# Kernel optimization log

Hardware: AMD Instinct MI355X
Metric: run time of the kernel (lower is better)

Reference implementation:

```python
import jax, jax.numpy as jnp
import numpy as np
from jax import lax

MASK_EPS = 1e-45  # matches torch (mask + 1e-45).log()

B, N, L, T = 32, 64, 64, 10
V, D, H = 50257, 256, 512


def setup_inputs() -> dict:
    key = jax.random.key(0)
    ks = jax.random.split(key, 10)
    s = 0.02
    return {
        "sents": jax.random.randint(ks[0], (B, N, L), 0, V),
        "titles": jax.random.randint(ks[1], (B, N, T), 0, V),
        "emb": jax.random.normal(ks[2], (V, D), jnp.float32) * s,
        "Wt": jax.random.normal(ks[3], (D, H), jnp.float32) * s,
        "bt": jnp.zeros((H,), jnp.float32),
        "W_ih": jax.random.normal(ks[4], (D, 3 * H), jnp.float32) * s,
        "W_hh": jax.random.normal(ks[5], (H, 3 * H), jnp.float32) * s,
        "b_ih": jnp.zeros((3 * H,), jnp.float32),
        "b_hh": jnp.zeros((3 * H,), jnp.float32),
        "W_att_in": jax.random.normal(ks[6], (H, H), jnp.float32) * s,
        "W_att_out": jax.random.normal(ks[7], (2 * H, H), jnp.float32) * s,
        "b_att_out": jnp.zeros((H,), jnp.float32),
    }


def reference(sents, titles, emb, Wt, bt, W_ih, W_hh, b_ih, b_hh,
              W_att_in, W_att_out, b_att_out):
    # embedding gather + per-sentence bag-of-words sum  [B,N,D]
    x = emb[sents].sum(axis=2)
    # title -> initial sentence-level hidden (t2h), titles[:,0,:-2] summed
    h0 = emb[titles[:, 0]].sum(axis=1) @ Wt + bt            # [B,H]

    def gru_step(h, xi):
        gi = xi @ W_ih + b_ih                               # [B,3H]
        gh = h @ W_hh + b_hh
        ir, iz, inn = jnp.split(gi, 3, axis=-1)
        hr, hz, hn = jnp.split(gh, 3, axis=-1)
        r = jax.nn.sigmoid(ir + hr)
        z = jax.nn.sigmoid(iz + hz)
        n = jnp.tanh(inn + r * hn)
        h_new = (1.0 - z) * n + z * h
        return h_new, h_new

    _, hs = lax.scan(gru_step, h0, jnp.swapaxes(x, 0, 1))   # [N,B,H]
    hs = jnp.swapaxes(hs, 0, 1)                             # [B,N,H]

    # GlobalAttention over the growing stack of hs with incremental mask
    # == causal attention over sentence hidden states
    q = hs @ W_att_in                                       # [B,N,H]
    align = jnp.einsum('bqh,bkh->bqk', q, hs)               # [B,N,N]
    causal = jnp.tril(jnp.ones((N, N), jnp.float32))
    align = align + jnp.log(causal + MASK_EPS)
    a = jax.nn.softmax(align, axis=-1)
    c = jnp.einsum('bqk,bkh->bqh', a, hs)                   # [B,N,H]
    attn_h = jnp.tanh(jnp.concatenate([c, hs], axis=-1) @ W_att_out + b_att_out)
    return attn_h
```

## Files before the change

### kernel.cpp

```cpp
#include <hip/hip_runtime.h>
#include <hip/hip_bf16.h>

constexpr int cB = 32, cN = 64, cL = 64, cT = 10, cD = 256, cH = 512, cH3 = 1536;
constexpr int cBN = cB * cN;
constexpr int cNP1 = cN + 1;

typedef __bf16 bf16x8 __attribute__((ext_vector_type(8)));
typedef float f32x4 __attribute__((ext_vector_type(4)));

__device__ __forceinline__ ushort f2bf(float f) {
  __hip_bfloat16 h = __float2bfloat16(f);
  return *reinterpret_cast<ushort*>(&h);
}

__global__ void k_embed_x(const int* __restrict__ sents, const float* __restrict__ emb,
                          ushort* __restrict__ xb) {
  __shared__ int idx[cL];
  int bn = blockIdx.x, t = threadIdx.x;
  if (t < cL) idx[t] = sents[bn * cL + t];
  __syncthreads();
  float acc = 0.f;
#pragma unroll 8
  for (int l = 0; l < cL; ++l) acc += emb[(long)idx[l] * cD + t];
  xb[bn * cD + t] = f2bf(acc);
}

__global__ void k_title(const int* __restrict__ titles, const float* __restrict__ emb,
                        float* __restrict__ tsum) {
  __shared__ int idx[cT];
  int b = blockIdx.x, t = threadIdx.x;
  if (t < cT) idx[t] = titles[b * cN * cT + t];
  __syncthreads();
  float acc = 0.f;
#pragma unroll
  for (int i = 0; i < cT; ++i) acc += emb[(long)idx[i] * cD + t];
  tsum[b * cD + t] = acc;
}

__global__ void k_h0(const float* __restrict__ tsum, const float* __restrict__ Wt,
                     const float* __restrict__ bt, float* __restrict__ hse) {
  int i = blockIdx.x * blockDim.x + threadIdx.x;
  int b = i >> 9, hh = i & (cH - 1);
  const float* ts = tsum + b * cD;
  float acc = bt[hh];
  for (int k = 0; k < cD; ++k) acc += ts[k] * Wt[(long)k * cH + hh];
  hse[(long)b * cNP1 * cH + hh] = acc;
}

__global__ void k_bti(const float* __restrict__ W, ushort* __restrict__ Bt) {
  __shared__ float tile[64][65];
  int col0 = blockIdx.x * 64, k0 = blockIdx.y * 64;
  int t = threadIdx.x;
  for (int i = t; i < 4096; i += 256) {
    int kr = i >> 6, cc = i & 63;
    tile[kr][cc] = W[(long)(k0 + kr) * cH3 + col0 + cc];
  }
  __syncthreads();
  for (int i = t; i < 4096; i += 256) {
    int cc = i >> 6, kr = i & 63;
    Bt[(long)(col0 + cc) * cD + k0 + kr] = f2bf(tile[kr][cc]);
  }
}

__global__ void k_bq(const float* __restrict__ W, ushort* __restrict__ Bt) {
  __shared__ float tile[64][65];
  int col0 = blockIdx.x * 64, k0 = blockIdx.y * 64;
  int t = threadIdx.x;
  for (int i = t; i < 4096; i += 256) {
    int kr = i >> 6, cc = i & 63;
    tile[kr][cc] = W[(long)(k0 + kr) * cH + col0 + cc];
  }
  __syncthreads();
  for (int i = t; i < 4096; i += 256) {
    int cc = i >> 6, kr = i & 63;
    Bt[(long)(col0 + cc) * cH + k0 + kr] = f2bf(tile[kr][cc]);
  }
}

__global__ void __launch_bounds__(256) k_gi_mfma(
    const ushort* __restrict__ xb, const ushort* __restrict__ Bt,
    const float* __restrict__ b_ih, float* __restrict__ gi) {
  __shared__ char lds[16384];
  int bn0 = blockIdx.x * 64, col0 = blockIdx.y * 64;
  int t = threadIdx.x;
  int w = t >> 6, lane = t & 63;
  f32x4 acc[4];
#pragma unroll
  for (int i = 0; i < 4; ++i) acc[i] = (f32x4){0.f, 0.f, 0.f, 0.f};
  int r = lane & 15, kg = lane >> 4;
  for (int kc = 0; kc < 4; ++kc) {
    int k0 = kc * 64;
#pragma unroll
    for (int p = 0; p < 2; ++p) {
      int i = t + p * 256;
      int row = i >> 3, ks = i & 7;
      float4 va = *(const float4*)(xb + (long)(bn0 + row) * cD + k0 + ks * 8);
      *(float4*)(lds + ((row * 128 + ks * 16) ^ ((row & 7) << 4))) = va;
      float4 vb = *(const float4*)(Bt + (long)(col0 + row) * cD + k0 + ks * 8);
      *(float4*)(lds + 8192 + ((row * 128 + ks * 16) ^ ((row & 7) << 4))) = vb;
    }
    __syncthreads();
#pragma unroll
    for (int s = 0; s < 2; ++s) {
      int arow = w * 16 + r;
      bf16x8 a = *(const bf16x8*)(lds + ((arow * 128 + s * 64 + kg * 16) ^ ((arow & 7) << 4)));
#pragma unroll
      for (int cf = 0; cf < 4; ++cf) {
        int bcol = cf * 16 + r;
        bf16x8 bb = *(const bf16x8*)(lds + 8192 +
                                     ((bcol * 128 + s * 64 + kg * 16) ^ ((bcol & 7) << 4)));
        acc[cf] = __builtin_amdgcn_mfma_f32_16x16x32_bf16(a, bb, acc[cf], 0, 0, 0);
      }
    }
    __syncthreads();
  }
  int rq = lane >> 4;
#pragma unroll
  for (int cf = 0; cf < 4; ++cf) {
    int col = col0 + cf * 16 + r;
    float bv = b_ih[col];
#pragma unroll
    for (int reg = 0; reg < 4; ++reg) {
      int row = bn0 + w * 16 + rq * 4 + reg;
      gi[(long)row * cH3 + col] = acc[cf][reg] + bv;
    }
  }
}

__global__ void __launch_bounds__(512, 1) k_gru_step(
    const float* __restrict__ gi, const float* __restrict__ W_hh,
    const float* __restrict__ b_hh, float* __restrict__ hse, int step) {
  __shared__ float part[512][13];
  int cg = blockIdx.x & 31;
  int bg = blockIdx.x >> 5;
  int t = threadIdx.x;

  float ir = 0.f, iz = 0.f, in_ = 0.f, bhr = 0.f, bhz = 0.f, bhn = 0.f, hold = 0.f;
  int e_bl = (t >> 4) & 3, e_cl = t & 15;
  if (t < 64) {
    int bb = bg * 4 + e_bl;
    int hh = cg * 16 + e_cl;
    long girow = ((long)bb * cN + step) * cH3;
    ir = gi[girow + hh];
    iz = gi[girow + hh + cH];
    in_ = gi[girow + hh + 2 * cH];
    bhr = b_hh[hh];
    bhz = b_hh[hh + cH];
    bhn = b_hh[hh + 2 * cH];
    hold = hse[((long)bb * cNP1 + step) * cH + hh];
  }

  int c4 = t & 3, b = (t >> 2) & 3, kp = t >> 4;
  int col0 = cg * 16 + c4 * 4;
  const float* hrow = hse + ((long)(bg * 4 + b) * cNP1 + step) * cH;
  int k0 = kp * 16;
  float4 h0 = *(const float4*)(hrow + k0);
  float4 h1 = *(const float4*)(hrow + k0 + 4);
  float4 h2 = *(const float4*)(hrow + k0 + 8);
  float4 h3 = *(const float4*)(hrow + k0 + 12);
  float ar[4] = {0, 0, 0, 0}, az[4] = {0, 0, 0, 0}, an[4] = {0, 0, 0, 0};
#define GRU_K(HV, KOFF)                                                         \
  {                                                                             \
    const float* wp = W_hh + (long)(k0 + (KOFF)) * cH3 + col0;                  \
    float4 wr = *(const float4*)(wp);                                           \
    float4 wz = *(const float4*)(wp + cH);                                      \
    float4 wn = *(const float4*)(wp + 2 * cH);                                  \
    ar[0] += (HV)*wr.x; ar[1] += (HV)*wr.y; ar[2] += (HV)*wr.z; ar[3] += (HV)*wr.w; \
    az[0] += (HV)*wz.x; az[1] += (HV)*wz.y; az[2] += (HV)*wz.z; az[3] += (HV)*wz.w; \
    an[0] += (HV)*wn.x; an[1] += (HV)*wn.y; an[2] += (HV)*wn.z; an[3] += (HV)*wn.w; \
  }
  GRU_K(h0.x, 0) GRU_K(h0.y, 1) GRU_K(h0.z, 2) GRU_K(h0.w, 3)
  GRU_K(h1.x, 4) GRU_K(h1.y, 5) GRU_K(h1.z, 6) GRU_K(h1.w, 7)
  GRU_K(h2.x, 8) GRU_K(h2.y, 9) GRU_K(h2.z, 10) GRU_K(h2.w, 11)
  GRU_K(h3.x, 12) GRU_K(h3.y, 13) GRU_K(h3.z, 14) GRU_K(h3.w, 15)
#undef GRU_K
#pragma unroll
  for (int j = 0; j < 4; ++j) {
    part[t][j] = ar[j];
    part[t][4 + j] = az[j];
    part[t][8 + j] = an[j];
  }
  __syncthreads();
  if (t < 64) {
    int c4f = e_cl >> 2, jf = e_cl & 3;
    float sr = 0.f, sz = 0.f, sn = 0.f;
#pragma unroll
    for (int p = 0; p < 32; ++p) {
      const float* pp = part[p * 16 + e_bl * 4 + c4f];
      sr += pp[jf];
      sz += pp[4 + jf];
      sn += pp[8 + jf];
    }
    int bb = bg * 4 + e_bl;
    int hh = cg * 16 + e_cl;
    float rr = 1.f / (1.f + __expf(-(ir + sr + bhr)));
    float zz = 1.f / (1.f + __expf(-(iz + sz + bhz)));
    float nn = tanhf(in_ + rr * (sn + bhn));
    hse[((long)bb * cNP1 + step + 1) * cH + hh] = (1.f - zz) * nn + zz * hold;
  }
}

__global__ void k_hscast(const float* __restrict__ hse, ushort* __restrict__ hsb,
                         ushort* __restrict__ catb) {
  int bn = blockIdx.x, t = threadIdx.x;
  int b = bn >> 6, n = bn & 63;
  float4 v = ((const float4*)(hse + ((long)b * cNP1 + 1 + n) * cH))[t];
  ushort4 o;
  o.x = f2bf(v.x); o.y = f2bf(v.y); o.z = f2bf(v.z); o.w = f2bf(v.w);
  *(ushort4*)(hsb + (long)bn * cH + t * 4) = o;
  *(ushort4*)(catb + (long)bn * 1024 + 512 + t * 4) = o;
}

__global__ void __launch_bounds__(256) k_q_mfma(
    const ushort* __restrict__ hsb, const ushort* __restrict__ Bt,
    float* __restrict__ q) {
  __shared__ char lds[16384];
  int bn0 = blockIdx.x * 64, col0 = blockIdx.y * 64;
  int t = threadIdx.x;
  int w = t >> 6, lane = t & 63;
  f32x4 acc[4];
#pragma unroll
  for (int i = 0; i < 4; ++i) acc[i] = (f32x4){0.f, 0.f, 0.f, 0.f};
  int r = lane & 15, kg = lane >> 4;
  for (int kc = 0; kc < 8; ++kc) {
    int k0 = kc * 64;
#pragma unroll
    for (int p = 0; p < 2; ++p) {
      int i = t + p * 256;
      int row = i >> 3, ks = i & 7;
      float4 va = *(const float4*)(hsb + (long)(bn0 + row) * cH + k0 + ks * 8);
      *(float4*)(lds + ((row * 128 + ks * 16) ^ ((row & 7) << 4))) = va;
      float4 vb = *(const float4*)(Bt + (long)(col0 + row) * cH + k0 + ks * 8);
      *(float4*)(lds + 8192 + ((row * 128 + ks * 16) ^ ((row & 7) << 4))) = vb;
    }
    __syncthreads();
#pragma unroll
    for (int s = 0; s < 2; ++s) {
      int arow = w * 16 + r;
      bf16x8 a = *(const bf16x8*)(lds + ((arow * 128 + s * 64 + kg * 16) ^ ((arow & 7) << 4)));
#pragma unroll
      for (int cf = 0; cf < 4; ++cf) {
        int bcol = cf * 16 + r;
        bf16x8 bb = *(const bf16x8*)(lds + 8192 +
                                     ((bcol * 128 + s * 64 + kg * 16) ^ ((bcol & 7) << 4)));
        acc[cf] = __builtin_amdgcn_mfma_f32_16x16x32_bf16(a, bb, acc[cf], 0, 0, 0);
      }
    }
    __syncthreads();
  }
  int rq = lane >> 4;
#pragma unroll
  for (int cf = 0; cf < 4; ++cf) {
    int col = col0 + cf * 16 + r;
#pragma unroll
    for (int reg = 0; reg < 4; ++reg) {
      int row = bn0 + w * 16 + rq * 4 + reg;
      q[(long)row * cH + col] = acc[cf][reg];
    }
  }
}

__global__ void k_attn2(const float* __restrict__ q, const float* __restrict__ hse,
                        ushort* __restrict__ catb) {
  __shared__ float qs[4][cH];
  __shared__ float part[256][5];
  __shared__ float aw[4][cN];
  int b = blockIdx.x, qg = blockIdx.y;
  int n0 = qg * 4;
  int kmax = n0 + 3;
  int t = threadIdx.x;
  for (int i = t; i < 4 * 128; i += 256) {
    int g = i >> 7, j = i & 127;
    ((float4*)qs[g])[j] = ((const float4*)(q + (long)(b * 64 + n0 + g) * cH))[j];
  }
  __syncthreads();
  int k = t & 63, p = t >> 6;
  float s0 = 0.f, s1 = 0.f, s2 = 0.f, s3 = 0.f;
  if (k <= kmax) {
    const float* hrow = hse + ((long)b * cNP1 + 1 + k) * cH + p * 128;
    const float* q0 = &qs[0][p * 128];
    const float* q1 = &qs[1][p * 128];
    const float* q2 = &qs[2][p * 128];
    const float* q3 = &qs[3][p * 128];
#pragma unroll 4
    for (int j = 0; j < 128; ++j) {
      float hv = hrow[j];
      s0 += q0[j] * hv;
      s1 += q1[j] * hv;
      s2 += q2[j] * hv;
      s3 += q3[j] * hv;
    }
  }
  part[t][0] = s0; part[t][1] = s1; part[t][2] = s2; part[t][3] = s3;
  __syncthreads();
  if (t < 64) {
#pragma unroll
    for (int g = 0; g < 4; ++g) {
      float sc = part[t][g] + part[t + 64][g] + part[t + 128][g] + part[t + 192][g];
      if (t > n0 + g) sc = -1e30f;
      float m = sc;
#pragma unroll
      for (int off = 32; off; off >>= 1) m = fmaxf(m, __shfl_xor(m, off));
      float e = __expf(sc - m);
      float sum = e;
#pragma unroll
      for (int off = 32; off; off >>= 1) sum += __shfl_xor(sum, off);
      aw[g][t] = e / sum;
    }
  }
  __syncthreads();
  float c0[4] = {0, 0, 0, 0}, c1[4] = {0, 0, 0, 0};
  for (int kk = 0; kk <= kmax; ++kk) {
    const float* hr = hse + ((long)b * cNP1 + 1 + kk) * cH;
    float h0 = hr[t], h1 = hr[t + 256];
#pragma unroll
    for (int g = 0; g < 4; ++g) {
      float a = aw[g][kk];
      c0[g] += a * h0;
      c1[g] += a * h1;
    }
  }
#pragma unroll
  for (int g = 0; g < 4; ++g) {
    long row = (long)(b * 64 + n0 + g) * 1024;
    catb[row + t] = f2bf(c0[g]);
    catb[row + t + 256] = f2bf(c1[g]);
  }
}

__global__ void k_bt(const float* __restrict__ W, ushort* __restrict__ Bt) {
  int t = threadIdx.x;
  int col = blockIdx.x * 2 + (t >> 7);
  int kg = t & 127;
  ushort u[8];
#pragma unroll
  for (int j = 0; j < 8; ++j) u[j] = f2bf(W[(long)(kg * 8 + j) * cH + col]);
  int4 o;
  o.x = (int)u[0] | ((int)u[1] << 16);
  o.y = (int)u[2] | ((int)u[3] << 16);
  o.z = (int)u[4] | ((int)u[5] << 16);
  o.w = (int)u[6] | ((int)u[7] << 16);
  *(int4*)(Bt + (long)col * 1024 + kg * 8) = o;
}

__global__ void __launch_bounds__(256) k_out_mfma(
    const ushort* __restrict__ cat, const ushort* __restrict__ Bt,
    const float* __restrict__ bias, float* __restrict__ out) {
  __shared__ char lds[16384];
  int bn0 = blockIdx.x * 64, col0 = blockIdx.y * 64;
  int t = threadIdx.x;
  int w = t >> 6, lane = t & 63;
  f32x4 acc[4];
#pragma unroll
  for (int i = 0; i < 4; ++i) acc[i] = (f32x4){0.f, 0.f, 0.f, 0.f};
  int r = lane & 15, kg = lane >> 4;
  for (int kc = 0; kc < 16; ++kc) {
    int k0 = kc * 64;
#pragma unroll
    for (int p = 0; p < 2; ++p) {
      int i = t + p * 256;
      int row = i >> 3, ks = i & 7;
      float4 va = *(const float4*)(cat + (long)(bn0 + row) * 1024 + k0 + ks * 8);
      *(float4*)(lds + ((row * 128 + ks * 16) ^ ((row & 7) << 4))) = va;
      float4 vb = *(const float4*)(Bt + (long)(col0 + row) * 1024 + k0 + ks * 8);
      *(float4*)(lds + 8192 + ((row * 128 + ks * 16) ^ ((row & 7) << 4))) = vb;
    }
    __syncthreads();
#pragma unroll
    for (int s = 0; s < 2; ++s) {
      int arow = w * 16 + r;
      bf16x8 a = *(const bf16x8*)(lds + ((arow * 128 + s * 64 + kg * 16) ^ ((arow & 7) << 4)));
#pragma unroll
      for (int cf = 0; cf < 4; ++cf) {
        int bcol = cf * 16 + r;
        bf16x8 bb = *(const bf16x8*)(lds + 8192 +
                                     ((bcol * 128 + s * 64 + kg * 16) ^ ((bcol & 7) << 4)));
        acc[cf] = __builtin_amdgcn_mfma_f32_16x16x32_bf16(a, bb, acc[cf], 0, 0, 0);
      }
    }
    __syncthreads();
  }
  int rq = lane >> 4;
#pragma unroll
  for (int cf = 0; cf < 4; ++cf) {
    int col = col0 + cf * 16 + r;
    float bv = bias[col];
#pragma unroll
    for (int reg = 0; reg < 4; ++reg) {
      int row = bn0 + w * 16 + rq * 4 + reg;
      out[(long)row * cH + col] = tanhf(acc[cf][reg] + bv);
    }
  }
}

extern "C" void kernel_launch(void* const* d_in, const int* in_sizes, int n_in,
                              void* d_out, int out_size, void* d_ws, size_t ws_size,
                              hipStream_t stream) {
  const int* sents = (const int*)d_in[0];
  const int* titles = (const int*)d_in[1];
  const float* emb = (const float*)d_in[2];
  const float* Wt = (const float*)d_in[3];
  const float* bt = (const float*)d_in[4];
  const float* W_ih = (const float*)d_in[5];
  const float* W_hh = (const float*)d_in[6];
  const float* b_ih = (const float*)d_in[7];
  const float* b_hh = (const float*)d_in[8];
  const float* W_att_in = (const float*)d_in[9];
  const float* W_att_out = (const float*)d_in[10];
  const float* b_att_out = (const float*)d_in[11];
  float* out = (float*)d_out;

  float* ws = (float*)d_ws;
  float* x = ws;
  float* tsum = x + (long)cBN * cD;
  float* gi = tsum + (long)cB * cD;
  float* hse = gi + (long)cBN * cH3;
  float* c = hse + (long)cB * cNP1 * cH;
  ushort* xb = (ushort*)(c + (long)cBN * cH);
  ushort* bti = xb + (long)cBN * cD;
  ushort* bq = bti + (long)cH3 * cD;
  float* q = gi;
  ushort* catb = (ushort*)(gi + (long)cBN * cH);
  ushort* Btb = catb + (long)cBN * 1024;
  ushort* hsb = Btb + (long)cH * 1024;

  k_embed_x<<<cBN, 256, 0, stream>>>(sents, emb, xb);
  k_title<<<cB, 256, 0, stream>>>(titles, emb, tsum);
  k_h0<<<(cB * cH) / 256, 256, 0, stream>>>(tsum, Wt, bt, hse);
  k_bti<<<dim3(24, 4), 256, 0, stream>>>(W_ih, bti);
  k_bq<<<dim3(8, 8), 256, 0, stream>>>(W_att_in, bq);
  k_gi_mfma<<<dim3(32, 24), 256, 0, stream>>>(xb, bti, b_ih, gi);
  for (int step = 0; step < cN; ++step)
    k_gru_step<<<256, 512, 0, stream>>>(gi, W_hh, b_hh, hse, step);
  k_hscast<<<cBN, 128, 0, stream>>>(hse, hsb, catb);
  k_q_mfma<<<dim3(32, 8), 256, 0, stream>>>(hsb, bq, q);
  k_attn2<<<dim3(cB, 16), 256, 0, stream>>>(q, hse, catb);
  k_bt<<<256, 256, 0, stream>>>(W_att_out, Btb);
  k_out_mfma<<<dim3(32, 8), 256, 0, stream>>>(catb, Btb, b_att_out, out);
}
```

Measured before the change: 461.7 us.

## Fuse GRU recurrence into one persistent kernel with fp16-packed W_hh dot2

```diff
diff --git a/kernel.cpp b/kernel.cpp
--- a/kernel.cpp
+++ b/kernel.cpp
@@ -7,10 +7,26 @@
 
 typedef __bf16 bf16x8 __attribute__((ext_vector_type(8)));
 typedef float f32x4 __attribute__((ext_vector_type(4)));
+typedef _Float16 h2t __attribute__((ext_vector_type(2)));
 
 __device__ __forceinline__ ushort f2bf(float f) {
   __hip_bfloat16 h = __float2bfloat16(f);
   return *reinterpret_cast<ushort*>(&h);
+}
+
+__device__ __forceinline__ unsigned pkh2(float a, float b) {
+  auto p = __builtin_amdgcn_cvt_pkrtz(a, b);
+  return __builtin_bit_cast(unsigned, p);
+}
+
+__device__ __forceinline__ float fdot2u(unsigned w, unsigned h, float acc) {
+#if __has_builtin(__builtin_amdgcn_fdot2)
+  return __builtin_amdgcn_fdot2(__builtin_bit_cast(h2t, w),
+                                __builtin_bit_cast(h2t, h), acc, false);
+#else
+  h2t a = __builtin_bit_cast(h2t, w), b = __builtin_bit_cast(h2t, h);
+  return acc + (float)a[0] * (float)b[0] + (float)a[1] * (float)b[1];
+#endif
 }
 
 __global__ void k_embed_x(const int* __restrict__ sents, const float* __restrict__ emb,
@@ -77,6 +93,18 @@
   }
 }
 
+__global__ void k_wpack(const float* __restrict__ W, uint4* __restrict__ Wp) {
+  int k8 = blockIdx.x, cg = blockIdx.y;
+  int t = threadIdx.x;
+  int cglob = cg * 256 + t;
+  int g = cglob >> 9, c = cglob & 511;
+  float v[8];
+#pragma unroll
+  for (int j = 0; j < 8; ++j) v[j] = W[(long)(k8 * 8 + j) * cH3 + cglob];
+  Wp[(g * 64 + k8) * 512 + c] = make_uint4(pkh2(v[0], v[1]), pkh2(v[2], v[3]),
+                                           pkh2(v[4], v[5]), pkh2(v[6], v[7]));
+}
+
 __global__ void __launch_bounds__(256) k_gi_mfma(
     const ushort* __restrict__ xb, const ushort* __restrict__ Bt,
     const float* __restrict__ b_ih, float* __restrict__ gi) {
@@ -127,76 +155,58 @@
   }
 }
 
-__global__ void __launch_bounds__(512, 1) k_gru_step(
-    const float* __restrict__ gi, const float* __restrict__ W_hh,
-    const float* __restrict__ b_hh, float* __restrict__ hse, int step) {
-  __shared__ float part[512][13];
-  int cg = blockIdx.x & 31;
-  int bg = blockIdx.x >> 5;
-  int t = threadIdx.x;
-
-  float ir = 0.f, iz = 0.f, in_ = 0.f, bhr = 0.f, bhz = 0.f, bhn = 0.f, hold = 0.f;
-  int e_bl = (t >> 4) & 3, e_cl = t & 15;
-  if (t < 64) {
-    int bb = bg * 4 + e_bl;
-    int hh = cg * 16 + e_cl;
-    long girow = ((long)bb * cN + step) * cH3;
-    ir = gi[girow + hh];
-    iz = gi[girow + hh + cH];
-    in_ = gi[girow + hh + 2 * cH];
-    bhr = b_hh[hh];
-    bhz = b_hh[hh + cH];
-    bhn = b_hh[hh + 2 * cH];
-    hold = hse[((long)bb * cNP1 + step) * cH + hh];
-  }
-
-  int c4 = t & 3, b = (t >> 2) & 3, kp = t >> 4;
-  int col0 = cg * 16 + c4 * 4;
-  const float* hrow = hse + ((long)(bg * 4 + b) * cNP1 + step) * cH;
-  int k0 = kp * 16;
-  float4 h0 = *(const float4*)(hrow + k0);
-  float4 h1 = *(const float4*)(hrow + k0 + 4);
-  float4 h2 = *(const float4*)(hrow + k0 + 8);
-  float4 h3 = *(const float4*)(hrow + k0 + 12);
-  float ar[4] = {0, 0, 0, 0}, az[4] = {0, 0, 0, 0}, an[4] = {0, 0, 0, 0};
-#define GRU_K(HV, KOFF)                                                         \
-  {                                                                             \
-    const float* wp = W_hh + (long)(k0 + (KOFF)) * cH3 + col0;                  \
-    float4 wr = *(const float4*)(wp);                                           \
-    float4 wz = *(const float4*)(wp + cH);                                      \
-    float4 wn = *(const float4*)(wp + 2 * cH);                                  \
-    ar[0] += (HV)*wr.x; ar[1] += (HV)*wr.y; ar[2] += (HV)*wr.z; ar[3] += (HV)*wr.w; \
-    az[0] += (HV)*wz.x; az[1] += (HV)*wz.y; az[2] += (HV)*wz.z; az[3] += (HV)*wz.w; \
-    an[0] += (HV)*wn.x; an[1] += (HV)*wn.y; an[2] += (HV)*wn.z; an[3] += (HV)*wn.w; \
-  }
-  GRU_K(h0.x, 0) GRU_K(h0.y, 1) GRU_K(h0.z, 2) GRU_K(h0.w, 3)
-  GRU_K(h1.x, 4) GRU_K(h1.y, 5) GRU_K(h1.z, 6) GRU_K(h1.w, 7)
-  GRU_K(h2.x, 8) GRU_K(h2.y, 9) GRU_K(h2.z, 10) GRU_K(h2.w, 11)
-  GRU_K(h3.x, 12) GRU_K(h3.y, 13) GRU_K(h3.z, 14) GRU_K(h3.w, 15)
-#undef GRU_K
-#pragma unroll
-  for (int j = 0; j < 4; ++j) {
-    part[t][j] = ar[j];
-    part[t][4 + j] = az[j];
-    part[t][8 + j] = an[j];
-  }
-  __syncthreads();
-  if (t < 64) {
-    int c4f = e_cl >> 2, jf = e_cl & 3;
-    float sr = 0.f, sz = 0.f, sn = 0.f;
-#pragma unroll
-    for (int p = 0; p < 32; ++p) {
-      const float* pp = part[p * 16 + e_bl * 4 + c4f];
-      sr += pp[jf];
-      sz += pp[4 + jf];
-      sn += pp[8 + jf];
-    }
-    int bb = bg * 4 + e_bl;
-    int hh = cg * 16 + e_cl;
-    float rr = 1.f / (1.f + __expf(-(ir + sr + bhr)));
-    float zz = 1.f / (1.f + __expf(-(iz + sz + bhz)));
-    float nn = tanhf(in_ + rr * (sn + bhn));
-    hse[((long)bb * cNP1 + step + 1) * cH + hh] = (1.f - zz) * nn + zz * hold;
+__global__ void __launch_bounds__(512) k_scan(
+    const float* __restrict__ gi, const uint4* __restrict__ Wp,
+    const float* __restrict__ b_hh, float* __restrict__ hse) {
+  __shared__ float hf[cH];
+  __shared__ uint4 hp4[64];
+  int b = blockIdx.x, c = threadIdx.x;
+  float bhr = b_hh[c], bhz = b_hh[c + cH], bhn = b_hh[c + 2 * cH];
+  float hcur = hse[(long)b * cNP1 * cH + c];
+  hf[c] = hcur;
+  __syncthreads();
+  if (c < 64) {
+    const float* s8 = &hf[c * 8];
+    hp4[c] = make_uint4(pkh2(s8[0], s8[1]), pkh2(s8[2], s8[3]),
+                        pkh2(s8[4], s8[5]), pkh2(s8[6], s8[7]));
+  }
+  __syncthreads();
+  const uint4* w0p = Wp + c;
+  const uint4* w1p = Wp + 64 * 512 + c;
+  const uint4* w2p = Wp + 128 * 512 + c;
+  for (int s = 0; s < cN; ++s) {
+    long girow = ((long)b * cN + s) * cH3;
+    float ir = gi[girow + c];
+    float iz = gi[girow + cH + c];
+    float inn = gi[girow + 2 * cH + c];
+    float a0 = 0.f, a1 = 0.f, z0 = 0.f, z1 = 0.f, n0 = 0.f, n1 = 0.f;
+#pragma unroll 4
+    for (int k8 = 0; k8 < 64; ++k8) {
+      uint4 hp = hp4[k8];
+      uint4 wr = w0p[k8 * 512];
+      uint4 wz = w1p[k8 * 512];
+      uint4 wn = w2p[k8 * 512];
+      a0 = fdot2u(wr.x, hp.x, a0); a1 = fdot2u(wr.y, hp.y, a1);
+      a0 = fdot2u(wr.z, hp.z, a0); a1 = fdot2u(wr.w, hp.w, a1);
+      z0 = fdot2u(wz.x, hp.x, z0); z1 = fdot2u(wz.y, hp.y, z1);
+      z0 = fdot2u(wz.z, hp.z, z0); z1 = fdot2u(wz.w, hp.w, z1);
+      n0 = fdot2u(wn.x, hp.x, n0); n1 = fdot2u(wn.y, hp.y, n1);
+      n0 = fdot2u(wn.z, hp.z, n0); n1 = fdot2u(wn.w, hp.w, n1);
+    }
+    float rr = 1.f / (1.f + __expf(-(ir + a0 + a1 + bhr)));
+    float zz = 1.f / (1.f + __expf(-(iz + z0 + z1 + bhz)));
+    float nn = tanhf(inn + rr * (n0 + n1 + bhn));
+    float hnew = (1.f - zz) * nn + zz * hcur;
+    hcur = hnew;
+    hse[((long)b * cNP1 + s + 1) * cH + c] = hnew;
+    hf[c] = hnew;
+    __syncthreads();
+    if (c < 64) {
+      const float* s8 = &hf[c * 8];
+      hp4[c] = make_uint4(pkh2(s8[0], s8[1]), pkh2(s8[2], s8[3]),
+                          pkh2(s8[4], s8[5]), pkh2(s8[6], s8[7]));
+    }
+    __syncthreads();
   }
 }
 
@@ -412,6 +422,7 @@
 
   float* ws = (float*)d_ws;
   float* x = ws;
+  uint4* Wp = (uint4*)x;
   float* tsum = x + (long)cBN * cD;
   float* gi = tsum + (long)cB * cD;
   float* hse = gi + (long)cBN * cH3;
@@ -429,9 +440,9 @@
   k_h0<<<(cB * cH) / 256, 256, 0, stream>>>(tsum, Wt, bt, hse);
   k_bti<<<dim3(24, 4), 256, 0, stream>>>(W_ih, bti);
   k_bq<<<dim3(8, 8), 256, 0, stream>>>(W_att_in, bq);
+  k_wpack<<<dim3(64, 6), 256, 0, stream>>>(W_hh, Wp);
   k_gi_mfma<<<dim3(32, 24), 256, 0, stream>>>(xb, bti, b_ih, gi);
-  for (int step = 0; step < cN; ++step)
-    k_gru_step<<<256, 512, 0, stream>>>(gi, W_hh, b_hh, hse, step);
+  k_scan<<<cB, 512, 0, stream>>>(gi, Wp, b_hh, hse);
   k_hscast<<<cBN, 128, 0, stream>>>(hse, hsb, catb);
   k_q_mfma<<<dim3(32, 8), 256, 0, stream>>>(hsb, bq, q);
   k_attn2<<<dim3(cB, 16), 256, 0, stream>>>(q, hse, catb);
```

New measurement: 833.2 us. 1.8x slower.

## Pack W_hh to fp16 and use dot2 instructions in GRU recurrence

Applied to the files above, without the earlier changes.

```diff
diff --git a/kernel.cpp b/kernel.cpp
--- a/kernel.cpp
+++ b/kernel.cpp
@@ -7,10 +7,26 @@
 
 typedef __bf16 bf16x8 __attribute__((ext_vector_type(8)));
 typedef float f32x4 __attribute__((ext_vector_type(4)));
+typedef _Float16 h2t __attribute__((ext_vector_type(2)));
 
 __device__ __forceinline__ ushort f2bf(float f) {
   __hip_bfloat16 h = __float2bfloat16(f);
   return *reinterpret_cast<ushort*>(&h);
+}
+
+__device__ __forceinline__ unsigned pkh2(float a, float b) {
+  auto p = __builtin_amdgcn_cvt_pkrtz(a, b);
+  return __builtin_bit_cast(unsigned, p);
+}
+
+__device__ __forceinline__ float fdot2u(unsigned w, unsigned h, float acc) {
+#if __has_builtin(__builtin_amdgcn_fdot2)
+  return __builtin_amdgcn_fdot2(__builtin_bit_cast(h2t, w),
+                                __builtin_bit_cast(h2t, h), acc, false);
+#else
+  h2t a = __builtin_bit_cast(h2t, w), b = __builtin_bit_cast(h2t, h);
+  return acc + (float)a[0] * (float)b[0] + (float)a[1] * (float)b[1];
+#endif
 }
 
 __global__ void k_embed_x(const int* __restrict__ sents, const float* __restrict__ emb,
@@ -77,6 +93,18 @@
   }
 }
 
+__global__ void k_wpack(const float* __restrict__ W, uint4* __restrict__ Wp) {
+  int k8 = blockIdx.x, cg = blockIdx.y;
+  int t = threadIdx.x;
+  int cglob = cg * 256 + t;
+  int g = cglob >> 9, c = cglob & 511;
+  float v[8];
+#pragma unroll
+  for (int j = 0; j < 8; ++j) v[j] = W[(long)(k8 * 8 + j) * cH3 + cglob];
+  Wp[(g * 64 + k8) * 512 + c] = make_uint4(pkh2(v[0], v[1]), pkh2(v[2], v[3]),
+                                           pkh2(v[4], v[5]), pkh2(v[6], v[7]));
+}
+
 __global__ void __launch_bounds__(256) k_gi_mfma(
     const ushort* __restrict__ xb, const ushort* __restrict__ Bt,
     const float* __restrict__ b_ih, float* __restrict__ gi) {
@@ -128,7 +156,7 @@
 }
 
 __global__ void __launch_bounds__(512, 1) k_gru_step(
-    const float* __restrict__ gi, const float* __restrict__ W_hh,
+    const float* __restrict__ gi, const uint4* __restrict__ Wp,
     const float* __restrict__ b_hh, float* __restrict__ hse, int step) {
   __shared__ float part[512][13];
   int cg = blockIdx.x & 31;
@@ -158,22 +186,29 @@
   float4 h1 = *(const float4*)(hrow + k0 + 4);
   float4 h2 = *(const float4*)(hrow + k0 + 8);
   float4 h3 = *(const float4*)(hrow + k0 + 12);
+  uint4 hp[2];
+  hp[0] = make_uint4(pkh2(h0.x, h0.y), pkh2(h0.z, h0.w), pkh2(h1.x, h1.y), pkh2(h1.z, h1.w));
+  hp[1] = make_uint4(pkh2(h2.x, h2.y), pkh2(h2.z, h2.w), pkh2(h3.x, h3.y), pkh2(h3.z, h3.w));
+
   float ar[4] = {0, 0, 0, 0}, az[4] = {0, 0, 0, 0}, an[4] = {0, 0, 0, 0};
-#define GRU_K(HV, KOFF)                                                         \
-  {                                                                             \
-    const float* wp = W_hh + (long)(k0 + (KOFF)) * cH3 + col0;                  \
-    float4 wr = *(const float4*)(wp);                                           \
-    float4 wz = *(const float4*)(wp + cH);                                      \
-    float4 wn = *(const float4*)(wp + 2 * cH);                                  \
-    ar[0] += (HV)*wr.x; ar[1] += (HV)*wr.y; ar[2] += (HV)*wr.z; ar[3] += (HV)*wr.w; \
-    az[0] += (HV)*wz.x; az[1] += (HV)*wz.y; az[2] += (HV)*wz.z; az[3] += (HV)*wz.w; \
-    an[0] += (HV)*wn.x; an[1] += (HV)*wn.y; an[2] += (HV)*wn.z; an[3] += (HV)*wn.w; \
-  }
-  GRU_K(h0.x, 0) GRU_K(h0.y, 1) GRU_K(h0.z, 2) GRU_K(h0.w, 3)
-  GRU_K(h1.x, 4) GRU_K(h1.y, 5) GRU_K(h1.z, 6) GRU_K(h1.w, 7)
-  GRU_K(h2.x, 8) GRU_K(h2.y, 9) GRU_K(h2.z, 10) GRU_K(h2.w, 11)
-  GRU_K(h3.x, 12) GRU_K(h3.y, 13) GRU_K(h3.z, 14) GRU_K(h3.w, 15)
-#undef GRU_K
+#pragma unroll
+  for (int i = 0; i < 2; ++i) {
+    int k8 = kp * 2 + i;
+    uint4 h4 = hp[i];
+#pragma unroll
+    for (int j = 0; j < 4; ++j) {
+      int col = col0 + j;
+      uint4 wr = Wp[(0 * 64 + k8) * 512 + col];
+      uint4 wz = Wp[(1 * 64 + k8) * 512 + col];
+      uint4 wn = Wp[(2 * 64 + k8) * 512 + col];
+      ar[j] = fdot2u(wr.x, h4.x, ar[j]); ar[j] = fdot2u(wr.y, h4.y, ar[j]);
+      ar[j] = fdot2u(wr.z, h4.z, ar[j]); ar[j] = fdot2u(wr.w, h4.w, ar[j]);
+      az[j] = fdot2u(wz.x, h4.x, az[j]); az[j] = fdot2u(wz.y, h4.y, az[j]);
+      az[j] = fdot2u(wz.z, h4.z, az[j]); az[j] = fdot2u(wz.w, h4.w, az[j]);
+      an[j] = fdot2u(wn.x, h4.x, an[j]); an[j] = fdot2u(wn.y, h4.y, an[j]);
+      an[j] = fdot2u(wn.z, h4.z, an[j]); an[j] = fdot2u(wn.w, h4.w, an[j]);
+    }
+  }
 #pragma unroll
   for (int j = 0; j < 4; ++j) {
     part[t][j] = ar[j];
@@ -412,6 +447,7 @@
 
   float* ws = (float*)d_ws;
   float* x = ws;
+  uint4* Wp = (uint4*)x;
   float* tsum = x + (long)cBN * cD;
   float* gi = tsum + (long)cB * cD;
   float* hse = gi + (long)cBN * cH3;
@@ -429,9 +465,10 @@
   k_h0<<<(cB * cH) / 256, 256, 0, stream>>>(tsum, Wt, bt, hse);
   k_bti<<<dim3(24, 4), 256, 0, stream>>>(W_ih, bti);
   k_bq<<<dim3(8, 8), 256, 0, stream>>>(W_att_in, bq);
+  k_wpack<<<dim3(64, 6), 256, 0, stream>>>(W_hh, Wp);
   k_gi_mfma<<<dim3(32, 24), 256, 0, stream>>>(xb, bti, b_ih, gi);
   for (int step = 0; step < cN; ++step)
-    k_gru_step<<<256, 512, 0, stream>>>(gi, W_hh, b_hh, hse, step);
+    k_gru_step<<<256, 512, 0, stream>>>(gi, Wp, b_hh, hse, step);
   k_hscast<<<cBN, 128, 0, stream>>>(hse, hsb, catb);
   k_q_mfma<<<dim3(32, 8), 256, 0, stream>>>(hsb, bq, q);
   k_attn2<<<dim3(cB, 16), 256, 0, stream>>>(q, hse, catb);
```

After: 460.9 us. About the same (-0.2%).
